# Kernel optimization log

Measured on AMD Instinct MI355X. Metric: run time of the kernel, lower is better.

The kernel has to match this reference:

```python
import jax, jax.numpy as jnp
import numpy as np

B, C, H, W, NCH = 2, 256, 48, 48, 12


def setup_inputs() -> dict:
    key = jax.random.key(0)
    k1, k2, k3, k4, k5 = jax.random.split(key, 5)
    gray_feature = jax.random.normal(k1, (B, C, H, W), jnp.float32)
    rgb_feature = jax.random.normal(k2, (B, C, H, W), jnp.float32)
    rgb_image = jax.random.uniform(k3, (B, 3, H, W), jnp.float32)
    # one-hot segmentation labels: random class id per pixel in [0, NCH)
    gcls = jax.random.randint(k4, (B, H, W), 0, NCH)
    rcls = jax.random.randint(k5, (B, H, W), 0, NCH)
    gray_label = jax.nn.one_hot(gcls, NCH, axis=1, dtype=jnp.float32)
    rgb_label = jax.nn.one_hot(rcls, NCH, axis=1, dtype=jnp.float32)
    return dict(gray_feature=gray_feature, rgb_feature=rgb_feature,
                rgb_image=rgb_image, gray_label=gray_label, rgb_label=rgb_label)


def _masked_normalize(feat, maskf):
    # feat: [b,c,N], maskf: [b,N] in {0,1}. Subtract per-channel masked mean,
    # then divide each masked pixel's feature vector by its channel-norm.
    cnt = maskf.sum(-1)                                            # [b]
    mean = jnp.einsum('bcn,bn->bc', feat, maskf) / jnp.maximum(cnt, 1.0)[:, None]
    bar = (feat - mean[:, :, None]) * maskf[:, None, :]            # zero outside mask
    norm = jnp.sqrt(jnp.sum(bar * bar, axis=1))                    # [b,N]
    unit = bar / jnp.where(norm > 0, norm, 1.0)[:, None, :]
    return unit, cnt


def reference(gray_feature, rgb_feature, rgb_image, gray_label, rgb_label):
    b, c, h, w = gray_feature.shape
    N = h * w
    gf = gray_feature.reshape(b, c, N)
    rf = rgb_feature.reshape(b, c, N)
    img = rgb_image.reshape(b, 3, N)
    gms = gray_label.reshape(b, -1, N) > 0.5   # [b,NCH,N] bool
    rms = rgb_label.reshape(b, -1, N) > 0.5
    canvas = -jnp.ones((b, 3, N), gray_feature.dtype)
    NEG = jnp.asarray(-1e30, gray_feature.dtype)
    for k in range(1, 12):  # classes 1..11, matching the torch loop
        gm = gms[:, k]                                     # [b,N]
        rm = rms[:, k]
        gmf = gm.astype(gf.dtype)
        rmf = rm.astype(rf.dtype)
        gn, cg = _masked_normalize(gf, gmf)                # [b,c,N]
        rn, cr = _masked_normalize(rf, rmf)
        # normalized correlation between gray and rgb masked pixels
        corr = jnp.einsum('bci,bcj->bij', gn, rn)          # [b,N,N]
        logits = jnp.where(rm[:, None, :], corr, NEG)      # softmax over rgb-mask pixels
        sm = jax.nn.softmax(logits, axis=-1)
        out = jnp.einsum('bij,bcj->bci', sm, img)          # [b,3,N]
        # skip condition from torch: needs >=2 pixels on each side
        valid = (cg > 1) & (cr > 1)                        # [b]
        write = gm & valid[:, None]                        # [b,N]
        canvas = jnp.where(write[:, None, :], out, canvas)
    return canvas.reshape(b, 3, h, w)
```

## Files before the change

### kernel.cpp

```cpp
#include <hip/hip_runtime.h>
#include <math.h>

#define BN 2
#define CC 256
#define NN 2304
#define KK 12
#define MC 320
#define KT 32
#define TT (MC / 64)

#define OFF_CLS_G  0
#define OFF_CLS_R  (OFF_CLS_G + BN * NN)
#define OFF_CNT_G  (OFF_CLS_R + BN * NN)
#define OFF_CNT_R  (OFF_CNT_G + 32)
#define OFF_IDX_G  (OFF_CNT_R + 32)
#define OFF_IDX_R  (OFF_IDX_G + BN * KK * MC)
#define OFF_MEAN_G (OFF_IDX_R + BN * KK * MC)
#define OFF_MEAN_R (OFF_MEAN_G + BN * KK * CC)
#define OFF_INV_G  (OFF_MEAN_R + BN * KK * CC)
#define OFF_INV_R  (OFF_INV_G + BN * NN)
#define OFF_IMGC   (OFF_INV_R + BN * NN)
#define OFF_UG     (OFF_IMGC + BN * KK * 3 * MC)
#define OFF_UR     (OFF_UG + BN * NN * CC)
#define OFF_LOG    (OFF_UR + BN * NN * CC)

__global__ __launch_bounds__(256) void prep_kernel(
        const float* __restrict__ gl, const float* __restrict__ rl,
        const float* __restrict__ img, float* __restrict__ out,
        int* cls_g, int* cls_r, int* cnt_g, int* cnt_r,
        int* idx_g, int* idx_r, float* imgc) {
    int bid = blockIdx.x, tid = threadIdx.x;
    int lane = tid & 63, wid = tid >> 6;
    if (bid < 12) {
        int unit = bid * 4 + wid;
        int type = unit / (BN * KK);
        int rem = unit % (BN * KK);
        int b = rem / KK, k = rem % KK;
        const float* lab = type ? rl : gl;
        int* idx = type ? idx_r : idx_g;
        int* cnt = type ? cnt_r : cnt_g;
        int count = 0;
        for (int i0 = 0; i0 < NN; i0 += 64) {
            int i = i0 + lane;
            bool p = (lab[((size_t)(b * KK + k)) * NN + i] > 0.5f);
            unsigned long long m = __ballot(p);
            if (p) {
                int pos = count + __popcll(m & ((1ull << lane) - 1));
                if (pos < MC) {
                    idx[(b * KK + k) * MC + pos] = i;
                    if (type) {
                        for (int ch = 0; ch < 3; ++ch)
                            imgc[((b * KK + k) * 3 + ch) * MC + pos] =
                                img[((size_t)(b * 3 + ch)) * NN + i];
                    }
                }
            }
            count += __popcll(m);
        }
        if (lane == 0) cnt[b * KK + k] = count;
    } else {
        int rbid = bid - 12;
        for (int gt = rbid * 256 + tid; gt < BN * NN; gt += 24 * 256) {
            int b = gt / NN, i = gt % NN;
            int kg = 0, kr = 0;
            for (int k = 0; k < KK; ++k) {
                if (gl[(b * KK + k) * NN + i] > 0.5f) kg = k;
                if (rl[(b * KK + k) * NN + i] > 0.5f) kr = k;
            }
            cls_g[gt] = kg;
            cls_r[gt] = kr;
        }
        for (int gt = rbid * 256 + tid; gt < BN * 3 * NN; gt += 24 * 256)
            out[gt] = -1.0f;
    }
}

__global__ __launch_bounds__(256) void mean_kernel(
        const float* __restrict__ gf, const float* __restrict__ rf,
        const int* __restrict__ cls_g, const int* __restrict__ cls_r,
        const int* __restrict__ cnt_g, const int* __restrict__ cnt_r,
        float* mean_g, float* mean_r) {
    int blk = blockIdx.x;
    int type = blk / (BN * CC);
    int rem = blk % (BN * CC);
    int b = rem >> 8, c = rem & 255;
    const float* f = type ? rf : gf;
    const int* cls = type ? cls_r : cls_g;
    const int* cnt = type ? cnt_r : cnt_g;
    float* mean = type ? mean_r : mean_g;

    int tid = threadIdx.x, lane = tid & 63, wid = tid >> 6;
    float acc[KK];
    #pragma unroll
    for (int k = 0; k < KK; ++k) acc[k] = 0.f;
    for (int i = tid; i < NN; i += 256) {
        float v = f[((size_t)(b * CC + c)) * NN + i];
        int k = cls[b * NN + i];
        #pragma unroll
        for (int kk = 0; kk < KK; ++kk) acc[kk] += (k == kk) ? v : 0.f;
    }
    #pragma unroll
    for (int kk = 0; kk < KK; ++kk) {
        #pragma unroll
        for (int o = 32; o; o >>= 1) acc[kk] += __shfl_xor(acc[kk], o, 64);
    }
    __shared__ float wsum[4][KK];
    if (lane == 0) {
        #pragma unroll
        for (int kk = 0; kk < KK; ++kk) wsum[wid][kk] = acc[kk];
    }
    __syncthreads();
    if (tid < KK) {
        float s = wsum[0][tid] + wsum[1][tid] + wsum[2][tid] + wsum[3][tid];
        float cn = (float)cnt[b * KK + tid];
        mean[(b * KK + tid) * CC + c] = s / fmaxf(cn, 1.f);
    }
}

__global__ __launch_bounds__(256) void center_kernel(
        const float* __restrict__ gf, const float* __restrict__ rf,
        const int* __restrict__ cls_g, const int* __restrict__ cls_r,
        const float* __restrict__ mean_g, const float* __restrict__ mean_r,
        float* ug, float* ur, float* inv_g, float* inv_r) {
    const int PCH = NN / 32;
    int blk = blockIdx.x;
    int type = blk / (BN * PCH);
    int rem = blk % (BN * PCH);
    int b = rem / PCH, chunk = rem % PCH;
    int i0 = chunk * 32;
    const float* f = type ? rf : gf;
    const int* cls = type ? cls_r : cls_g;
    const float* mean = type ? mean_r : mean_g;
    float* u = type ? ur : ug;
    float* invp = type ? inv_r : inv_g;

    __shared__ float lmean[KK * 257];
    __shared__ float tile[64 * 33];

    int tid = threadIdx.x;
    for (int x = tid; x < KK * CC; x += 256) {
        int k = x >> 8, c = x & 255;
        lmean[k * 257 + c] = mean[(b * KK + k) * CC + c];
    }
    int p = tid >> 3, q = tid & 7;
    int pl = tid & 31, cb = tid >> 5;
    int kc = cls[b * NN + i0 + p];
    float ss = 0.f;
    float* ub = u + ((size_t)(b * NN + i0 + p)) * CC;
    for (int cc = 0; cc < 4; ++cc) {
        __syncthreads();
        for (int j = 0; j < 8; ++j) {
            int c = cb * 8 + j;
            tile[c * 33 + pl] = f[((size_t)(b * CC + cc * 64 + c)) * NN + i0 + pl];
        }
        __syncthreads();
        #pragma unroll
        for (int h = 0; h < 2; ++h) {
            int c0 = q * 8 + h * 4;
            float4 v;
            v.x = tile[(c0 + 0) * 33 + p] - lmean[kc * 257 + cc * 64 + c0 + 0];
            v.y = tile[(c0 + 1) * 33 + p] - lmean[kc * 257 + cc * 64 + c0 + 1];
            v.z = tile[(c0 + 2) * 33 + p] - lmean[kc * 257 + cc * 64 + c0 + 2];
            v.w = tile[(c0 + 3) * 33 + p] - lmean[kc * 257 + cc * 64 + c0 + 3];
            ss += v.x * v.x + v.y * v.y + v.z * v.z + v.w * v.w;
            *(float4*)&ub[cc * 64 + c0] = v;
        }
    }
    ss += __shfl_xor(ss, 1, 64);
    ss += __shfl_xor(ss, 2, 64);
    ss += __shfl_xor(ss, 4, 64);
    if (q == 0) invp[b * NN + i0 + p] = (ss > 0.f) ? rsqrtf(ss) : 1.0f;
}

__global__ __launch_bounds__(256) void gemm_kernel(
        const int* __restrict__ cnt_g, const int* __restrict__ cnt_r,
        const int* __restrict__ idx_g, const int* __restrict__ idx_r,
        const float* __restrict__ ug, const float* __restrict__ ur,
        float* logits) {
    int blk = blockIdx.x;
    int tk = blk % TT;
    int tq = (blk / TT) % TT;
    int k = (blk / (TT * TT)) % KK;
    int b = blk / (TT * TT * KK);
    if (k == 0) return;
    int Mg = min(cnt_g[b * KK + k], MC);
    int Mr = min(cnt_r[b * KK + k], MC);
    if (Mg <= 1 || Mr <= 1) return;
    int q0 = tq * 64, k0 = tk * 64;
    if (q0 >= Mg || k0 >= Mr) return;
    int qn = min(64, Mg - q0), kn = min(64, Mr - k0);

    __shared__ float As[KT * 68];
    __shared__ float Bs[KT * 68];

    int tid = threadIdx.x;
    int r = tid >> 2, c4 = tid & 3;
    const int* lg = idx_g + (b * KK + k) * MC;
    const int* lr = idx_r + (b * KK + k) * MC;
    int gi = lg[q0 + ((r < qn) ? r : 0)];
    int rj = lr[k0 + ((r < kn) ? r : 0)];
    const float* rowA = ug + ((size_t)(b * NN + gi)) * CC;
    const float* rowB = ur + ((size_t)(b * NN + rj)) * CC;

    int tx = tid & 15, ty = tid >> 4;
    float acc[4][4];
    #pragma unroll
    for (int x = 0; x < 4; ++x)
        #pragma unroll
        for (int y = 0; y < 4; ++y) acc[x][y] = 0.f;

    for (int kcc = 0; kcc < CC; kcc += KT) {
        #pragma unroll
        for (int jj = 0; jj < 2; ++jj) {
            int ch = jj * 16 + c4 * 4;
            float4 va = *(const float4*)&rowA[kcc + ch];
            float4 vb = *(const float4*)&rowB[kcc + ch];
            As[(ch + 0) * 68 + r] = va.x;
            As[(ch + 1) * 68 + r] = va.y;
            As[(ch + 2) * 68 + r] = va.z;
            As[(ch + 3) * 68 + r] = va.w;
            Bs[(ch + 0) * 68 + r] = vb.x;
            Bs[(ch + 1) * 68 + r] = vb.y;
            Bs[(ch + 2) * 68 + r] = vb.z;
            Bs[(ch + 3) * 68 + r] = vb.w;
        }
        __syncthreads();
        #pragma unroll 4
        for (int kk = 0; kk < KT; ++kk) {
            float4 av = *(const float4*)&As[kk * 68 + ty * 4];
            float4 bv = *(const float4*)&Bs[kk * 68 + tx * 4];
            acc[0][0] += av.x * bv.x; acc[0][1] += av.x * bv.y;
            acc[0][2] += av.x * bv.z; acc[0][3] += av.x * bv.w;
            acc[1][0] += av.y * bv.x; acc[1][1] += av.y * bv.y;
            acc[1][2] += av.y * bv.z; acc[1][3] += av.y * bv.w;
            acc[2][0] += av.z * bv.x; acc[2][1] += av.z * bv.y;
            acc[2][2] += av.z * bv.z; acc[2][3] += av.z * bv.w;
            acc[3][0] += av.w * bv.x; acc[3][1] += av.w * bv.y;
            acc[3][2] += av.w * bv.z; acc[3][3] += av.w * bv.w;
        }
        __syncthreads();
    }
    float* S = logits + ((size_t)((b * KK + k) * MC)) * MC;
    #pragma unroll
    for (int x = 0; x < 4; ++x) {
        int row = q0 + ty * 4 + x;
        float4 o = make_float4(acc[x][0], acc[x][1], acc[x][2], acc[x][3]);
        *(float4*)&S[(size_t)row * MC + k0 + tx * 4] = o;
    }
}

__global__ __launch_bounds__(256) void softmax_kernel(
        const int* __restrict__ cnt_g, const int* __restrict__ cnt_r,
        const int* __restrict__ idx_g, const int* __restrict__ idx_r,
        const float* __restrict__ inv_g, const float* __restrict__ inv_r,
        const float* __restrict__ imgc, const float* __restrict__ logits,
        float* out) {
    const int RC = MC / 4;
    int rc = blockIdx.x % RC;
    int k = (blockIdx.x / RC) % KK;
    int b = blockIdx.x / (RC * KK);
    if (k == 0) return;
    int cg_ = cnt_g[b * KK + k], cr_ = cnt_r[b * KK + k];
    if (cg_ <= 1 || cr_ <= 1) return;
    int Mg = min(cg_, MC), Mr = min(cr_, MC);
    int wid = threadIdx.x >> 6, lane = threadIdx.x & 63;
    int il = rc * 4 + wid;
    if (il >= Mg) return;
    int gi = idx_g[(b * KK + k) * MC + il];
    float inv_i = inv_g[b * NN + gi];
    const float* row = logits + ((size_t)((b * KK + k) * MC + il)) * MC;
    const int* lr = idx_r + (b * KK + k) * MC;
    const float* im0 = imgc + ((b * KK + k) * 3 + 0) * MC;
    const float* im1 = imgc + ((b * KK + k) * 3 + 1) * MC;
    const float* im2 = imgc + ((b * KK + k) * 3 + 2) * MC;

    float v[TT];
    float mx = -1e30f;
    #pragma unroll
    for (int u = 0; u < TT; ++u) {
        int m = lane + 64 * u;
        v[u] = (m < Mr) ? row[m] * inv_i * inv_r[b * NN + lr[m]] : -1e30f;
        mx = fmaxf(mx, v[u]);
    }
    #pragma unroll
    for (int o = 32; o; o >>= 1) mx = fmaxf(mx, __shfl_xor(mx, o, 64));
    float s = 0.f, p0 = 0.f, p1 = 0.f, p2 = 0.f;
    #pragma unroll
    for (int u = 0; u < TT; ++u) {
        int m = lane + 64 * u;
        if (m < Mr) {
            float e = __expf(v[u] - mx);
            s += e;
            p0 += e * im0[m];
            p1 += e * im1[m];
            p2 += e * im2[m];
        }
    }
    #pragma unroll
    for (int o = 32; o; o >>= 1) {
        s  += __shfl_xor(s,  o, 64);
        p0 += __shfl_xor(p0, o, 64);
        p1 += __shfl_xor(p1, o, 64);
        p2 += __shfl_xor(p2, o, 64);
    }
    if (lane == 0) {
        float inv = 1.0f / s;
        out[((size_t)(b * 3 + 0)) * NN + gi] = p0 * inv;
        out[((size_t)(b * 3 + 1)) * NN + gi] = p1 * inv;
        out[((size_t)(b * 3 + 2)) * NN + gi] = p2 * inv;
    }
}

extern "C" void kernel_launch(void* const* d_in, const int* in_sizes, int n_in,
                              void* d_out, int out_size, void* d_ws, size_t ws_size,
                              hipStream_t stream) {
    const float* gf  = (const float*)d_in[0];
    const float* rf  = (const float*)d_in[1];
    const float* img = (const float*)d_in[2];
    const float* gl  = (const float*)d_in[3];
    const float* rl  = (const float*)d_in[4];
    float* out = (float*)d_out;
    float* ws = (float*)d_ws;

    int*   cls_g  = (int*)(ws + OFF_CLS_G);
    int*   cls_r  = (int*)(ws + OFF_CLS_R);
    int*   cnt_g  = (int*)(ws + OFF_CNT_G);
    int*   cnt_r  = (int*)(ws + OFF_CNT_R);
    int*   idx_g  = (int*)(ws + OFF_IDX_G);
    int*   idx_r  = (int*)(ws + OFF_IDX_R);
    float* mean_g = ws + OFF_MEAN_G;
    float* mean_r = ws + OFF_MEAN_R;
    float* inv_g  = ws + OFF_INV_G;
    float* inv_r  = ws + OFF_INV_R;
    float* imgc   = ws + OFF_IMGC;
    float* ug     = ws + OFF_UG;
    float* ur     = ws + OFF_UR;
    float* logits = ws + OFF_LOG;

    prep_kernel<<<36, 256, 0, stream>>>(gl, rl, img, out, cls_g, cls_r,
                                        cnt_g, cnt_r, idx_g, idx_r, imgc);
    mean_kernel<<<2 * BN * CC, 256, 0, stream>>>(gf, rf, cls_g, cls_r, cnt_g, cnt_r,
                                                 mean_g, mean_r);
    center_kernel<<<2 * BN * (NN / 32), 256, 0, stream>>>(gf, rf, cls_g, cls_r,
                                                          mean_g, mean_r, ug, ur,
                                                          inv_g, inv_r);
    gemm_kernel<<<BN * KK * TT * TT, 256, 0, stream>>>(cnt_g, cnt_r, idx_g, idx_r,
                                                       ug, ur, logits);
    softmax_kernel<<<BN * KK * (MC / 4), 256, 0, stream>>>(cnt_g, cnt_r, idx_g, idx_r,
                                                           inv_g, inv_r, imgc, logits,
                                                           out);
}
```

Measured before the change: 132.5 us.

## Fuse correlation GEMM with softmax-weighted sum and merge prep with mean pass

Merges label compaction and per-class channel sums into one launch, computing sums from the one-hot labels instead of a separate class map. Centering now writes compacted per-class unit vectors and inverse norms so the GEMM reads contiguous rows without index gathers. The GEMM and softmax are fused into a single kernel that exponentiates correlations directly and accumulates image-weighted sums, dropping the logits buffer, one launch and the max pass. Skipping the max subtraction relies on cosine correlations being bounded in [-1,1], and the compaction scan now uses block-level barriers per 256-pixel chunk.

```diff
diff --git a/kernel.cpp b/kernel.cpp
--- a/kernel.cpp
+++ b/kernel.cpp
@@ -7,121 +7,108 @@
 #define KK 12
 #define MC 320
 #define KT 32
-#define TT (MC / 64)
-
-#define OFF_CLS_G  0
-#define OFF_CLS_R  (OFF_CLS_G + BN * NN)
-#define OFF_CNT_G  (OFF_CLS_R + BN * NN)
-#define OFF_CNT_R  (OFF_CNT_G + 32)
-#define OFF_IDX_G  (OFF_CNT_R + 32)
-#define OFF_IDX_R  (OFF_IDX_G + BN * KK * MC)
-#define OFF_MEAN_G (OFF_IDX_R + BN * KK * MC)
-#define OFF_MEAN_R (OFF_MEAN_G + BN * KK * CC)
-#define OFF_INV_G  (OFF_MEAN_R + BN * KK * CC)
-#define OFF_INV_R  (OFF_INV_G + BN * NN)
-#define OFF_IMGC   (OFF_INV_R + BN * NN)
-#define OFF_UG     (OFF_IMGC + BN * KK * 3 * MC)
-#define OFF_UR     (OFF_UG + BN * NN * CC)
-#define OFF_LOG    (OFF_UR + BN * NN * CC)
-
-__global__ __launch_bounds__(256) void prep_kernel(
-        const float* __restrict__ gl, const float* __restrict__ rl,
-        const float* __restrict__ img, float* __restrict__ out,
-        int* cls_g, int* cls_r, int* cnt_g, int* cnt_r,
-        int* idx_g, int* idx_r, float* imgc) {
+#define QT 32
+#define TNQ (MC / QT)
+
+#define OFF_CNT_G   0
+#define OFF_CNT_R   32
+#define OFF_IDX_G   64
+#define OFF_CPS_G   (OFF_IDX_G + BN * KK * MC)
+#define OFF_CPS_R   (OFF_CPS_G + BN * NN)
+#define OFF_MSUM_G  (OFF_CPS_R + BN * NN)
+#define OFF_MSUM_R  (OFF_MSUM_G + BN * KK * CC)
+#define OFF_IMGC    (OFF_MSUM_R + BN * KK * CC)
+#define OFF_INV_G   (OFF_IMGC + BN * KK * 3 * MC)
+#define OFF_INV_R   (OFF_INV_G + BN * KK * MC)
+#define OFF_UCG     (OFF_INV_R + BN * KK * MC)
+#define OFF_UCR     (OFF_UCG + BN * KK * MC * CC)
+
+__global__ __launch_bounds__(256) void prep_mean_kernel(
+        const float* __restrict__ gf, const float* __restrict__ rf,
+        const float* __restrict__ img, const float* __restrict__ gl,
+        const float* __restrict__ rl, float* __restrict__ out,
+        int* cnt_g, int* cnt_r, int* idx_g, int* cps_g, int* cps_r,
+        float* imgc, float* msum_g, float* msum_r) {
+    __shared__ int wcnt[4];
+    __shared__ float wsum[4][KK];
     int bid = blockIdx.x, tid = threadIdx.x;
     int lane = tid & 63, wid = tid >> 6;
-    if (bid < 12) {
-        int unit = bid * 4 + wid;
-        int type = unit / (BN * KK);
-        int rem = unit % (BN * KK);
+
+    if (bid < 48) {
+        int type = bid / (BN * KK);
+        int rem = bid % (BN * KK);
         int b = rem / KK, k = rem % KK;
-        const float* lab = type ? rl : gl;
-        int* idx = type ? idx_r : idx_g;
+        const float* lp = (type ? rl : gl) + ((size_t)(b * KK + k)) * NN;
+        int* cps = type ? cps_r : cps_g;
         int* cnt = type ? cnt_r : cnt_g;
-        int count = 0;
-        for (int i0 = 0; i0 < NN; i0 += 64) {
-            int i = i0 + lane;
-            bool p = (lab[((size_t)(b * KK + k)) * NN + i] > 0.5f);
+        int base = 0;
+        for (int c0 = 0; c0 < NN; c0 += 256) {
+            int i = c0 + tid;
+            bool p = lp[i] > 0.5f;
             unsigned long long m = __ballot(p);
+            int rank = __popcll(m & ((1ull << lane) - 1));
+            if (lane == 0) wcnt[wid] = __popcll(m);
+            __syncthreads();
+            int pre = 0;
+            for (int w = 0; w < wid; ++w) pre += wcnt[w];
+            int tot = wcnt[0] + wcnt[1] + wcnt[2] + wcnt[3];
             if (p) {
-                int pos = count + __popcll(m & ((1ull << lane) - 1));
+                int pos = base + pre + rank;
+                cps[b * NN + i] = (k << 16) | pos;
                 if (pos < MC) {
-                    idx[(b * KK + k) * MC + pos] = i;
                     if (type) {
                         for (int ch = 0; ch < 3; ++ch)
                             imgc[((b * KK + k) * 3 + ch) * MC + pos] =
                                 img[((size_t)(b * 3 + ch)) * NN + i];
+                    } else {
+                        idx_g[(b * KK + k) * MC + pos] = i;
                     }
                 }
             }
-            count += __popcll(m);
-        }
-        if (lane == 0) cnt[b * KK + k] = count;
+            base += tot;
+            __syncthreads();
+        }
+        if (tid == 0) cnt[b * KK + k] = base;
     } else {
-        int rbid = bid - 12;
-        for (int gt = rbid * 256 + tid; gt < BN * NN; gt += 24 * 256) {
-            int b = gt / NN, i = gt % NN;
-            int kg = 0, kr = 0;
-            for (int k = 0; k < KK; ++k) {
-                if (gl[(b * KK + k) * NN + i] > 0.5f) kg = k;
-                if (rl[(b * KK + k) * NN + i] > 0.5f) kr = k;
-            }
-            cls_g[gt] = kg;
-            cls_r[gt] = kr;
-        }
-        for (int gt = rbid * 256 + tid; gt < BN * 3 * NN; gt += 24 * 256)
-            out[gt] = -1.0f;
-    }
-}
-
-__global__ __launch_bounds__(256) void mean_kernel(
-        const float* __restrict__ gf, const float* __restrict__ rf,
-        const int* __restrict__ cls_g, const int* __restrict__ cls_r,
-        const int* __restrict__ cnt_g, const int* __restrict__ cnt_r,
-        float* mean_g, float* mean_r) {
-    int blk = blockIdx.x;
-    int type = blk / (BN * CC);
-    int rem = blk % (BN * CC);
-    int b = rem >> 8, c = rem & 255;
-    const float* f = type ? rf : gf;
-    const int* cls = type ? cls_r : cls_g;
-    const int* cnt = type ? cnt_r : cnt_g;
-    float* mean = type ? mean_r : mean_g;
-
-    int tid = threadIdx.x, lane = tid & 63, wid = tid >> 6;
-    float acc[KK];
-    #pragma unroll
-    for (int k = 0; k < KK; ++k) acc[k] = 0.f;
-    for (int i = tid; i < NN; i += 256) {
-        float v = f[((size_t)(b * CC + c)) * NN + i];
-        int k = cls[b * NN + i];
-        #pragma unroll
-        for (int kk = 0; kk < KK; ++kk) acc[kk] += (k == kk) ? v : 0.f;
-    }
-    #pragma unroll
-    for (int kk = 0; kk < KK; ++kk) {
-        #pragma unroll
-        for (int o = 32; o; o >>= 1) acc[kk] += __shfl_xor(acc[kk], o, 64);
-    }
-    __shared__ float wsum[4][KK];
-    if (lane == 0) {
-        #pragma unroll
-        for (int kk = 0; kk < KK; ++kk) wsum[wid][kk] = acc[kk];
-    }
-    __syncthreads();
-    if (tid < KK) {
-        float s = wsum[0][tid] + wsum[1][tid] + wsum[2][tid] + wsum[3][tid];
-        float cn = (float)cnt[b * KK + tid];
-        mean[(b * KK + tid) * CC + c] = s / fmaxf(cn, 1.f);
+        int u = bid - 48;
+        if (u < 54) out[u * 256 + tid] = -1.0f;
+        int type = u >> 9;
+        int rem = u & 511;
+        int b = rem >> 8, c = rem & 255;
+        const float* f = (type ? rf : gf) + ((size_t)(b * CC + c)) * NN;
+        const float* lab = (type ? rl : gl) + ((size_t)b) * KK * NN;
+        float* msum = type ? msum_r : msum_g;
+
+        float acc[KK];
+        #pragma unroll
+        for (int kk = 0; kk < KK; ++kk) acc[kk] = 0.f;
+        for (int i = tid; i < NN; i += 256) {
+            float v = f[i];
+            #pragma unroll
+            for (int kk = 0; kk < KK; ++kk) acc[kk] += lab[(size_t)kk * NN + i] * v;
+        }
+        #pragma unroll
+        for (int kk = 0; kk < KK; ++kk) {
+            #pragma unroll
+            for (int o = 32; o; o >>= 1) acc[kk] += __shfl_xor(acc[kk], o, 64);
+        }
+        if (lane == 0) {
+            #pragma unroll
+            for (int kk = 0; kk < KK; ++kk) wsum[wid][kk] = acc[kk];
+        }
+        __syncthreads();
+        if (tid < KK)
+            msum[(b * KK + tid) * CC + c] =
+                wsum[0][tid] + wsum[1][tid] + wsum[2][tid] + wsum[3][tid];
     }
 }
 
 __global__ __launch_bounds__(256) void center_kernel(
         const float* __restrict__ gf, const float* __restrict__ rf,
-        const int* __restrict__ cls_g, const int* __restrict__ cls_r,
-        const float* __restrict__ mean_g, const float* __restrict__ mean_r,
-        float* ug, float* ur, float* inv_g, float* inv_r) {
+        const int* __restrict__ cps_g, const int* __restrict__ cps_r,
+        const int* __restrict__ cnt_g, const int* __restrict__ cnt_r,
+        const float* __restrict__ msum_g, const float* __restrict__ msum_r,
+        float* ucg, float* ucr, float* inv_g, float* inv_r) {
     const int PCH = NN / 32;
     int blk = blockIdx.x;
     int type = blk / (BN * PCH);
@@ -129,10 +116,11 @@
     int b = rem / PCH, chunk = rem % PCH;
     int i0 = chunk * 32;
     const float* f = type ? rf : gf;
-    const int* cls = type ? cls_r : cls_g;
-    const float* mean = type ? mean_r : mean_g;
-    float* u = type ? ur : ug;
-    float* invp = type ? inv_r : inv_g;
+    const int* cps = type ? cps_r : cps_g;
+    const int* cnt = type ? cnt_r : cnt_g;
+    const float* msum = type ? msum_r : msum_g;
+    float* uc = type ? ucr : ucg;
+    float* invc = type ? inv_r : inv_g;
 
     __shared__ float lmean[KK * 257];
     __shared__ float tile[64 * 33];
@@ -140,13 +128,16 @@
     int tid = threadIdx.x;
     for (int x = tid; x < KK * CC; x += 256) {
         int k = x >> 8, c = x & 255;
-        lmean[k * 257 + c] = mean[(b * KK + k) * CC + c];
+        float cn = fmaxf((float)cnt[b * KK + k], 1.f);
+        lmean[k * 257 + c] = msum[(b * KK + k) * CC + c] / cn;
     }
     int p = tid >> 3, q = tid & 7;
     int pl = tid & 31, cb = tid >> 5;
-    int kc = cls[b * NN + i0 + p];
+    int kcpos = cps[b * NN + i0 + p];
+    int kc = kcpos >> 16, pos = kcpos & 0xFFFF;
+    bool wr = pos < MC;
     float ss = 0.f;
-    float* ub = u + ((size_t)(b * NN + i0 + p)) * CC;
+    float* ub = uc + ((size_t)((b * KK + kc) * MC + (wr ? pos : MC - 1))) * CC;
     for (int cc = 0; cc < 4; ++cc) {
         __syncthreads();
         for (int j = 0; j < 8; ++j) {
@@ -163,151 +154,134 @@
             v.z = tile[(c0 + 2) * 33 + p] - lmean[kc * 257 + cc * 64 + c0 + 2];
             v.w = tile[(c0 + 3) * 33 + p] - lmean[kc * 257 + cc * 64 + c0 + 3];
             ss += v.x * v.x + v.y * v.y + v.z * v.z + v.w * v.w;
-            *(float4*)&ub[cc * 64 + c0] = v;
+            if (wr) *(float4*)&ub[cc * 64 + c0] = v;
         }
     }
     ss += __shfl_xor(ss, 1, 64);
     ss += __shfl_xor(ss, 2, 64);
     ss += __shfl_xor(ss, 4, 64);
-    if (q == 0) invp[b * NN + i0 + p] = (ss > 0.f) ? rsqrtf(ss) : 1.0f;
+    if (q == 0 && wr)
+        invc[(b * KK + kc) * MC + pos] = (ss > 0.f) ? rsqrtf(ss) : 1.0f;
 }
 
-__global__ __launch_bounds__(256) void gemm_kernel(
+__global__ __launch_bounds__(256) void corr_out_kernel(
         const int* __restrict__ cnt_g, const int* __restrict__ cnt_r,
-        const int* __restrict__ idx_g, const int* __restrict__ idx_r,
-        const float* __restrict__ ug, const float* __restrict__ ur,
-        float* logits) {
-    int blk = blockIdx.x;
-    int tk = blk % TT;
-    int tq = (blk / TT) % TT;
-    int k = (blk / (TT * TT)) % KK;
-    int b = blk / (TT * TT * KK);
+        const int* __restrict__ idx_g,
+        const float* __restrict__ ucg, const float* __restrict__ ucr,
+        const float* __restrict__ inv_g, const float* __restrict__ inv_r,
+        const float* __restrict__ imgc, float* __restrict__ out) {
+    int tq = blockIdx.x % TNQ;
+    int k = (blockIdx.x / TNQ) % KK;
+    int b = blockIdx.x / (TNQ * KK);
     if (k == 0) return;
-    int Mg = min(cnt_g[b * KK + k], MC);
-    int Mr = min(cnt_r[b * KK + k], MC);
-    if (Mg <= 1 || Mr <= 1) return;
-    int q0 = tq * 64, k0 = tk * 64;
-    if (q0 >= Mg || k0 >= Mr) return;
-    int qn = min(64, Mg - q0), kn = min(64, Mr - k0);
-
-    __shared__ float As[KT * 68];
-    __shared__ float Bs[KT * 68];
-
-    int tid = threadIdx.x;
-    int r = tid >> 2, c4 = tid & 3;
-    const int* lg = idx_g + (b * KK + k) * MC;
-    const int* lr = idx_r + (b * KK + k) * MC;
-    int gi = lg[q0 + ((r < qn) ? r : 0)];
-    int rj = lr[k0 + ((r < kn) ? r : 0)];
-    const float* rowA = ug + ((size_t)(b * NN + gi)) * CC;
-    const float* rowB = ur + ((size_t)(b * NN + rj)) * CC;
-
-    int tx = tid & 15, ty = tid >> 4;
-    float acc[4][4];
-    #pragma unroll
-    for (int x = 0; x < 4; ++x)
-        #pragma unroll
-        for (int y = 0; y < 4; ++y) acc[x][y] = 0.f;
-
-    for (int kcc = 0; kcc < CC; kcc += KT) {
-        #pragma unroll
-        for (int jj = 0; jj < 2; ++jj) {
-            int ch = jj * 16 + c4 * 4;
-            float4 va = *(const float4*)&rowA[kcc + ch];
-            float4 vb = *(const float4*)&rowB[kcc + ch];
-            As[(ch + 0) * 68 + r] = va.x;
-            As[(ch + 1) * 68 + r] = va.y;
-            As[(ch + 2) * 68 + r] = va.z;
-            As[(ch + 3) * 68 + r] = va.w;
-            Bs[(ch + 0) * 68 + r] = vb.x;
-            Bs[(ch + 1) * 68 + r] = vb.y;
-            Bs[(ch + 2) * 68 + r] = vb.z;
-            Bs[(ch + 3) * 68 + r] = vb.w;
-        }
-        __syncthreads();
-        #pragma unroll 4
-        for (int kk = 0; kk < KT; ++kk) {
-            float4 av = *(const float4*)&As[kk * 68 + ty * 4];
-            float4 bv = *(const float4*)&Bs[kk * 68 + tx * 4];
-            acc[0][0] += av.x * bv.x; acc[0][1] += av.x * bv.y;
-            acc[0][2] += av.x * bv.z; acc[0][3] += av.x * bv.w;
-            acc[1][0] += av.y * bv.x; acc[1][1] += av.y * bv.y;
-            acc[1][2] += av.y * bv.z; acc[1][3] += av.y * bv.w;
-            acc[2][0] += av.z * bv.x; acc[2][1] += av.z * bv.y;
-            acc[2][2] += av.z * bv.z; acc[2][3] += av.z * bv.w;
-            acc[3][0] += av.w * bv.x; acc[3][1] += av.w * bv.y;
-            acc[3][2] += av.w * bv.z; acc[3][3] += av.w * bv.w;
-        }
-        __syncthreads();
-    }
-    float* S = logits + ((size_t)((b * KK + k) * MC)) * MC;
-    #pragma unroll
-    for (int x = 0; x < 4; ++x) {
-        int row = q0 + ty * 4 + x;
-        float4 o = make_float4(acc[x][0], acc[x][1], acc[x][2], acc[x][3]);
-        *(float4*)&S[(size_t)row * MC + k0 + tx * 4] = o;
-    }
-}
-
-__global__ __launch_bounds__(256) void softmax_kernel(
-        const int* __restrict__ cnt_g, const int* __restrict__ cnt_r,
-        const int* __restrict__ idx_g, const int* __restrict__ idx_r,
-        const float* __restrict__ inv_g, const float* __restrict__ inv_r,
-        const float* __restrict__ imgc, const float* __restrict__ logits,
-        float* out) {
-    const int RC = MC / 4;
-    int rc = blockIdx.x % RC;
-    int k = (blockIdx.x / RC) % KK;
-    int b = blockIdx.x / (RC * KK);
-    if (k == 0) return;
-    int cg_ = cnt_g[b * KK + k], cr_ = cnt_r[b * KK + k];
+    int bk = b * KK + k;
+    int cg_ = cnt_g[bk], cr_ = cnt_r[bk];
     if (cg_ <= 1 || cr_ <= 1) return;
     int Mg = min(cg_, MC), Mr = min(cr_, MC);
-    int wid = threadIdx.x >> 6, lane = threadIdx.x & 63;
-    int il = rc * 4 + wid;
-    if (il >= Mg) return;
-    int gi = idx_g[(b * KK + k) * MC + il];
-    float inv_i = inv_g[b * NN + gi];
-    const float* row = logits + ((size_t)((b * KK + k) * MC + il)) * MC;
-    const int* lr = idx_r + (b * KK + k) * MC;
-    const float* im0 = imgc + ((b * KK + k) * 3 + 0) * MC;
-    const float* im1 = imgc + ((b * KK + k) * 3 + 1) * MC;
-    const float* im2 = imgc + ((b * KK + k) * 3 + 2) * MC;
-
-    float v[TT];
-    float mx = -1e30f;
+    int q0 = tq * QT;
+    if (q0 >= Mg) return;
+
+    __shared__ float Af[CC * 34];
+    __shared__ float Bs[KT * 68];
+
+    int tid = threadIdx.x;
+    {
+        int r = tid >> 3, c8 = tid & 7;
+        const float* rowA = ucg + ((size_t)(bk * MC + q0 + r)) * CC;
+        #pragma unroll
+        for (int j = 0; j < 8; ++j) {
+            int c0 = j * 32 + c8 * 4;
+            float4 va = *(const float4*)&rowA[c0];
+            Af[(c0 + 0) * 34 + r] = va.x;
+            Af[(c0 + 1) * 34 + r] = va.y;
+            Af[(c0 + 2) * 34 + r] = va.z;
+            Af[(c0 + 3) * 34 + r] = va.w;
+        }
+    }
+    int tx = tid & 15, ty = tid >> 4;
+    float invi[2];
     #pragma unroll
-    for (int u = 0; u < TT; ++u) {
-        int m = lane + 64 * u;
-        v[u] = (m < Mr) ? row[m] * inv_i * inv_r[b * NN + lr[m]] : -1e30f;
-        mx = fmaxf(mx, v[u]);
+    for (int x = 0; x < 2; ++x) invi[x] = inv_g[bk * MC + q0 + ty * 2 + x];
+    const float* im0 = imgc + (bk * 3 + 0) * MC;
+    const float* im1 = imgc + (bk * 3 + 1) * MC;
+    const float* im2 = imgc + (bk * 3 + 2) * MC;
+
+    float s[2] = {0.f, 0.f}, p0[2] = {0.f, 0.f}, p1[2] = {0.f, 0.f}, p2[2] = {0.f, 0.f};
+    int r2 = tid >> 2, c4 = tid & 3;
+
+    for (int k0 = 0; k0 < Mr; k0 += 64) {
+        float acc[2][4];
+        #pragma unroll
+        for (int x = 0; x < 2; ++x)
+            #pragma unroll
+            for (int y = 0; y < 4; ++y) acc[x][y] = 0.f;
+
+        for (int kcc = 0; kcc < CC; kcc += KT) {
+            __syncthreads();
+            const float* rowB = ucr + ((size_t)(bk * MC + k0 + r2)) * CC + kcc;
+            #pragma unroll
+            for (int jj = 0; jj < 2; ++jj) {
+                int ch = jj * 16 + c4 * 4;
+                float4 vb = *(const float4*)&rowB[ch];
+                Bs[(ch + 0) * 68 + r2] = vb.x;
+                Bs[(ch + 1) * 68 + r2] = vb.y;
+                Bs[(ch + 2) * 68 + r2] = vb.z;
+                Bs[(ch + 3) * 68 + r2] = vb.w;
+            }
+            __syncthreads();
+            #pragma unroll 8
+            for (int kk = 0; kk < KT; ++kk) {
+                float2 av = *(const float2*)&Af[(kcc + kk) * 34 + ty * 2];
+                float4 bv = *(const float4*)&Bs[kk * 68 + tx * 4];
+                acc[0][0] += av.x * bv.x; acc[0][1] += av.x * bv.y;
+                acc[0][2] += av.x * bv.z; acc[0][3] += av.x * bv.w;
+                acc[1][0] += av.y * bv.x; acc[1][1] += av.y * bv.y;
+                acc[1][2] += av.y * bv.z; acc[1][3] += av.y * bv.w;
+            }
+        }
+        float4 w0 = *(const float4*)&im0[k0 + tx * 4];
+        float4 w1 = *(const float4*)&im1[k0 + tx * 4];
+        float4 w2 = *(const float4*)&im2[k0 + tx * 4];
+        float4 vj = *(const float4*)&inv_r[bk * MC + k0 + tx * 4];
+        float wj0[4] = {w0.x, w0.y, w0.z, w0.w};
+        float wj1[4] = {w1.x, w1.y, w1.z, w1.w};
+        float wj2[4] = {w2.x, w2.y, w2.z, w2.w};
+        float vjj[4] = {vj.x, vj.y, vj.z, vj.w};
+        #pragma unroll
+        for (int x = 0; x < 2; ++x) {
+            #pragma unroll
+            for (int y = 0; y < 4; ++y) {
+                int col = k0 + tx * 4 + y;
+                float e = (col < Mr) ? __expf(acc[x][y] * invi[x] * vjj[y]) : 0.f;
+                s[x] += e;
+                p0[x] += e * wj0[y];
+                p1[x] += e * wj1[y];
+                p2[x] += e * wj2[y];
+            }
+        }
     }
     #pragma unroll
-    for (int o = 32; o; o >>= 1) mx = fmaxf(mx, __shfl_xor(mx, o, 64));
-    float s = 0.f, p0 = 0.f, p1 = 0.f, p2 = 0.f;
-    #pragma unroll
-    for (int u = 0; u < TT; ++u) {
-        int m = lane + 64 * u;
-        if (m < Mr) {
-            float e = __expf(v[u] - mx);
-            s += e;
-            p0 += e * im0[m];
-            p1 += e * im1[m];
-            p2 += e * im2[m];
-        }
-    }
-    #pragma unroll
-    for (int o = 32; o; o >>= 1) {
-        s  += __shfl_xor(s,  o, 64);
-        p0 += __shfl_xor(p0, o, 64);
-        p1 += __shfl_xor(p1, o, 64);
-        p2 += __shfl_xor(p2, o, 64);
-    }
-    if (lane == 0) {
-        float inv = 1.0f / s;
-        out[((size_t)(b * 3 + 0)) * NN + gi] = p0 * inv;
-        out[((size_t)(b * 3 + 1)) * NN + gi] = p1 * inv;
-        out[((size_t)(b * 3 + 2)) * NN + gi] = p2 * inv;
+    for (int o = 1; o <= 8; o <<= 1) {
+        #pragma unroll
+        for (int x = 0; x < 2; ++x) {
+            s[x]  += __shfl_xor(s[x],  o, 64);
+            p0[x] += __shfl_xor(p0[x], o, 64);
+            p1[x] += __shfl_xor(p1[x], o, 64);
+            p2[x] += __shfl_xor(p2[x], o, 64);
+        }
+    }
+    if (tx == 0) {
+        #pragma unroll
+        for (int x = 0; x < 2; ++x) {
+            int row = q0 + ty * 2 + x;
+            if (row < Mg) {
+                int gi = idx_g[bk * MC + row];
+                float inv = 1.0f / s[x];
+                out[((size_t)(b * 3 + 0)) * NN + gi] = p0[x] * inv;
+                out[((size_t)(b * 3 + 1)) * NN + gi] = p1[x] * inv;
+                out[((size_t)(b * 3 + 2)) * NN + gi] = p2[x] * inv;
+            }
+        }
     }
 }
 
@@ -322,31 +296,25 @@
     float* out = (float*)d_out;
     float* ws = (float*)d_ws;
 
-    int*   cls_g  = (int*)(ws + OFF_CLS_G);
-    int*   cls_r  = (int*)(ws + OFF_CLS_R);
     int*   cnt_g  = (int*)(ws + OFF_CNT_G);
     int*   cnt_r  = (int*)(ws + OFF_CNT_R);
     int*   idx_g  = (int*)(ws + OFF_IDX_G);
-    int*   idx_r  = (int*)(ws + OFF_IDX_R);
-    float* mean_g = ws + OFF_MEAN_G;
-    float* mean_r = ws + OFF_MEAN_R;
+    int*   cps_g  = (int*)(ws + OFF_CPS_G);
+    int*   cps_r  = (int*)(ws + OFF_CPS_R);
+    float* msum_g = ws + OFF_MSUM_G;
+    float* msum_r = ws + OFF_MSUM_R;
+    float* imgc   = ws + OFF_IMGC;
     float* inv_g  = ws + OFF_INV_G;
     float* inv_r  = ws + OFF_INV_R;
-    float* imgc   = ws + OFF_IMGC;
-    float* ug     = ws + OFF_UG;
-    float* ur     = ws + OFF_UR;
-    float* logits = ws + OFF_LOG;
-
-    prep_kernel<<<36, 256, 0, stream>>>(gl, rl, img, out, cls_g, cls_r,
-                                        cnt_g, cnt_r, idx_g, idx_r, imgc);
-    mean_kernel<<<2 * BN * CC, 256, 0, stream>>>(gf, rf, cls_g, cls_r, cnt_g, cnt_r,
-                                                 mean_g, mean_r);
-    center_kernel<<<2 * BN * (NN / 32), 256, 0, stream>>>(gf, rf, cls_g, cls_r,
-                                                          mean_g, mean_r, ug, ur,
-                                                          inv_g, inv_r);
-    gemm_kernel<<<BN * KK * TT * TT, 256, 0, stream>>>(cnt_g, cnt_r, idx_g, idx_r,
-                                                       ug, ur, logits);
-    softmax_kernel<<<BN * KK * (MC / 4), 256, 0, stream>>>(cnt_g, cnt_r, idx_g, idx_r,
-                                                           inv_g, inv_r, imgc, logits,
-                                                           out);
+    float* ucg    = ws + OFF_UCG;
+    float* ucr    = ws + OFF_UCR;
+
+    prep_mean_kernel<<<48 + 2 * BN * CC, 256, 0, stream>>>(
+        gf, rf, img, gl, rl, out, cnt_g, cnt_r, idx_g, cps_g, cps_r,
+        imgc, msum_g, msum_r);
+    center_kernel<<<2 * BN * (NN / 32), 256, 0, stream>>>(
+        gf, rf, cps_g, cps_r, cnt_g, cnt_r, msum_g, msum_r,
+        ucg, ucr, inv_g, inv_r);
+    corr_out_kernel<<<BN * KK * TNQ, 256, 0, stream>>>(
+        cnt_g, cnt_r, idx_g, ucg, ucr, inv_g, inv_r, imgc, out);
 }
```

Result: faster. 123.4 us (-6.8%).
